# Performance work log

Hardware: AMD Instinct MI355X
Metric: run time of the kernel (lower is better)

## Reference

```python
import jax, jax.numpy as jnp
import numpy as np

VOCAB, HID, ADIM, B = 20, 128, 3, 32
NP, EP, NM, EM = 50000, 800000, 50000, 800000
IN_DIM = VOCAB + 3  # one-hot residues + 3D pos


def _gcn_conv(x, edge_index, W, b, n):
    # PyG GCNConv: h = XW; add self-loops; sym-normalized scatter-add; + bias
    h = x @ W
    loop = jnp.arange(n, dtype=edge_index.dtype)
    src = jnp.concatenate([edge_index[0], loop])
    dst = jnp.concatenate([edge_index[1], loop])
    deg = jax.ops.segment_sum(jnp.ones_like(dst, dtype=h.dtype), dst, num_segments=n)
    dinv = jnp.where(deg > 0, jax.lax.rsqrt(deg), 0.0)
    norm = dinv[src] * dinv[dst]  # [E+N]
    msg = h[src] * norm[:, None]  # [E+N, HID] dominant memory traffic
    return jax.ops.segment_sum(msg, dst, num_segments=n) + b


def _mean_pool(x, batch, nb):
    s = jax.ops.segment_sum(x, batch, num_segments=nb)
    c = jax.ops.segment_sum(jnp.ones((x.shape[0],), x.dtype), batch, num_segments=nb)
    return s / jnp.maximum(c, 1.0)[:, None]


def setup_inputs() -> dict:
    key = jax.random.key(0)
    ks = jax.random.split(key, 32)
    p = lambda k, shp: jax.random.normal(k, shp, dtype=jnp.float32) * 0.02
    inp = {
        "protein_residue": jax.random.randint(ks[0], (NP,), 0, VOCAB, dtype=jnp.int32),
        "protein_pos": jax.random.normal(ks[1], (NP, 3), dtype=jnp.float32),
        "protein_edge_index": jax.random.randint(ks[2], (2, EP), 0, NP, dtype=jnp.int32),
        "protein_batch": jnp.sort(jax.random.randint(ks[3], (NP,), 0, B, dtype=jnp.int32)),
        "molecule_residue": jax.random.randint(ks[4], (NM,), 0, VOCAB, dtype=jnp.int32),
        "molecule_pos": jax.random.normal(ks[5], (NM, 3), dtype=jnp.float32),
        "molecule_edge_index": jax.random.randint(ks[6], (2, EM), 0, NM, dtype=jnp.int32),
        "molecule_batch": jnp.sort(jax.random.randint(ks[7], (NM,), 0, B, dtype=jnp.int32)),
        "t": jax.random.randint(ks[8], (B,), 0, 1000, dtype=jnp.int32),
        "noisy_action": jax.random.normal(ks[9], (NM, ADIM), dtype=jnp.float32),
        # GCN params
        "Wp1": p(ks[10], (IN_DIM, HID)), "bp1": jnp.zeros((HID,), jnp.float32),
        "Wp2": p(ks[11], (HID, HID)),   "bp2": jnp.zeros((HID,), jnp.float32),
        "Wm1": p(ks[12], (IN_DIM, HID)), "bm1": jnp.zeros((HID,), jnp.float32),
        "Wm2": p(ks[13], (HID, HID)),   "bm2": jnp.zeros((HID,), jnp.float32),
        # timestep MLP
        "Wt1": p(ks[14], (1, HID)),   "bt1": jnp.zeros((HID,), jnp.float32),
        "Wt2": p(ks[15], (HID, HID)), "bt2": jnp.zeros((HID,), jnp.float32),
        # noise predictor: in = 2*HID + ADIM + HID = 387
        "Wn1": p(ks[16], (2 * HID + ADIM + HID, HID)), "bn1": jnp.zeros((HID,), jnp.float32),
        "Wn2": p(ks[17], (HID, ADIM)), "bn2": jnp.zeros((ADIM,), jnp.float32),
    }
    return inp


def reference(protein_residue, protein_pos, protein_edge_index, protein_batch,
              molecule_residue, molecule_pos, molecule_edge_index, molecule_batch,
              t, noisy_action,
              Wp1, bp1, Wp2, bp2, Wm1, bm1, Wm2, bm2,
              Wt1, bt1, Wt2, bt2, Wn1, bn1, Wn2, bn2):
    # protein branch
    x_p = jnp.concatenate([jax.nn.one_hot(protein_residue, VOCAB, dtype=jnp.float32), protein_pos], axis=1)
    x_p = jax.nn.relu(_gcn_conv(x_p, protein_edge_index, Wp1, bp1, NP))
    x_p = jax.nn.relu(_gcn_conv(x_p, protein_edge_index, Wp2, bp2, NP))
    protein_emb = _mean_pool(x_p, protein_batch, B)  # [B, HID]
    # molecule branch
    x_m = jnp.concatenate([jax.nn.one_hot(molecule_residue, VOCAB, dtype=jnp.float32), molecule_pos], axis=1)
    x_m = jax.nn.relu(_gcn_conv(x_m, molecule_edge_index, Wm1, bm1, NM))
    x_m = jax.nn.relu(_gcn_conv(x_m, molecule_edge_index, Wm2, bm2, NM))
    # timestep embedding
    t_emb = jax.nn.relu(t[:, None].astype(jnp.float32) @ Wt1 + bt1) @ Wt2 + bt2  # [B, HID]
    # gather pooled embeddings per molecule node, concat, MLP
    feat = jnp.concatenate([x_m, protein_emb[molecule_batch], t_emb[molecule_batch], noisy_action], axis=1)
    return jax.nn.relu(feat @ Wn1 + bn1) @ Wn2 + bn2  # [NM, ADIM]
```

## Files before the change

### kernel.cpp

```cpp
#include <hip/hip_runtime.h>
#include <hip/hip_bf16.h>

#define HID 128
#define BSH 7
#define CSRCAP 4096
#define PCHUNK 4096
#define HCHUNK 16384

typedef __attribute__((ext_vector_type(8))) short short8v;
typedef __attribute__((ext_vector_type(4))) float f32x4;

#if defined(__has_builtin)
#if __has_builtin(__builtin_amdgcn_cvt_f32_fp8) && __has_builtin(__builtin_amdgcn_cvt_pk_fp8_f32)
#define HAVE_HW_FP8 1
#endif
#endif

__device__ __forceinline__ float4 f4fma(float a, float4 x, float4 y) {
    y.x += a * x.x; y.y += a * x.y; y.z += a * x.z; y.w += a * x.w; return y;
}
__device__ __forceinline__ unsigned f2bf2(float lo, float hi) {
    unsigned ul = __float_as_uint(lo), uh = __float_as_uint(hi);
    ul = (ul + 0x7FFF + ((ul >> 16) & 1)) >> 16;
    uh = (uh + 0x7FFF + ((uh >> 16) & 1)) & 0xFFFF0000u;
    return ul | uh;
}
__device__ __forceinline__ unsigned short f2bf1(float v) {
    unsigned u = __float_as_uint(v);
    u = (u + 0x7FFF + ((u >> 16) & 1)) >> 16;
    return (unsigned short)u;
}
__device__ __forceinline__ float bflo(unsigned u) { return __uint_as_float(u << 16); }
__device__ __forceinline__ float bfhi(unsigned u) { return __uint_as_float(u & 0xFFFF0000u); }
__device__ __forceinline__ float bf2f(unsigned short b) {
    return __uint_as_float(((unsigned)b) << 16);
}
__device__ __forceinline__ short8v zero8() {
    short8v z = {0, 0, 0, 0, 0, 0, 0, 0};
    return z;
}

#ifndef HAVE_HW_FP8
__device__ __forceinline__ unsigned fp8enc_pos(float a) {
    if (a >= 448.f) return 0x7Eu;
    if (a < 0.0009765625f) return 0u;
    unsigned b = __float_as_uint(a);
    int e = (int)(b >> 23) - 127;
    if (e >= -6) {
        unsigned r = b + 0x7FFFFu + ((b >> 20) & 1u);
        e = (int)(r >> 23) - 127;
        unsigned m = (r >> 20) & 7u;
        return ((unsigned)(e + 7) << 3) | m;
    } else {
        int m = (int)(a * 512.f + 0.5f);
        return (unsigned)m;
    }
}
__device__ __forceinline__ float fp8dec1(unsigned u7) {
    float fn = __uint_as_float((u7 + 0x3C0u) << 20);
    float fs = (float)u7 * 0.001953125f;
    return u7 >= 8 ? fn : fs;
}
#endif

__device__ __forceinline__ unsigned char enc1(float a) {
#ifdef HAVE_HW_FP8
    return (unsigned char)(__builtin_amdgcn_cvt_pk_fp8_f32(a, 0.f, 0, false) & 0xff);
#else
    return (unsigned char)fp8enc_pos(a);
#endif
}
__device__ __forceinline__ void dec4(unsigned x, float* v) {
#ifdef HAVE_HW_FP8
    v[0] = __builtin_amdgcn_cvt_f32_fp8((int)x, 0);
    v[1] = __builtin_amdgcn_cvt_f32_fp8((int)x, 1);
    v[2] = __builtin_amdgcn_cvt_f32_fp8((int)x, 2);
    v[3] = __builtin_amdgcn_cvt_f32_fp8((int)x, 3);
#else
    v[0] = fp8dec1(x & 0xffu);         v[1] = fp8dec1((x >> 8) & 0xffu);
    v[2] = fp8dec1((x >> 16) & 0xffu); v[3] = fp8dec1(x >> 24);
#endif
}
__device__ __forceinline__ void dec16(uint4 u, float* v) {
    dec4(u.x, v); dec4(u.y, v + 4); dec4(u.z, v + 8); dec4(u.w, v + 12);
}

__global__ __launch_bounds__(256) void k_bhist(const int* __restrict__ d1, int e1,
        const int* __restrict__ d2, int e2, int base2,
        int* __restrict__ bktcnt, long etot) {
    __shared__ int hist[1024];
    int tid = threadIdx.x;
    for (int b = tid; b < 1024; b += 256) hist[b] = 0;
    __syncthreads();
    long start = (long)blockIdx.x * HCHUNK;
    long end = start + HCHUNK; if (end > etot) end = etot;
    for (long i = start + tid; i < end; i += 256) {
        int d = (i < e1) ? d1[i] : d2[i - e1] + base2;
        atomicAdd(&hist[d >> BSH], 1);
    }
    __syncthreads();
    for (int b = tid; b < 1024; b += 256)
        if (hist[b]) atomicAdd(&bktcnt[b], hist[b]);
}

__global__ void k_bscan(const int* __restrict__ bktcnt, int* __restrict__ bofs,
                        int* __restrict__ bcur) {
    __shared__ int s[1024];
    int tid = threadIdx.x;
    int v = bktcnt[tid];
    s[tid] = v; __syncthreads();
    for (int o = 1; o < 1024; o <<= 1) {
        int t = (tid >= o) ? s[tid - o] : 0;
        __syncthreads();
        s[tid] += t;
        __syncthreads();
    }
    int ex = s[tid] - v;
    bofs[tid] = ex;
    bcur[tid] = ex;
    if (tid == 1023) bofs[1024] = s[1023];
}

__global__ __launch_bounds__(256) void k_part(
        const int* __restrict__ s1, const int* __restrict__ d1, int e1,
        const int* __restrict__ s2, const int* __restrict__ d2, int e2, int base2,
        int* __restrict__ bcur, int* __restrict__ pedge, int nb, long etot) {
    __shared__ int hist[1024];
    __shared__ int lofs[1024];
    __shared__ int gb[1024];
    __shared__ int ps[256];
    __shared__ int stage[PCHUNK];
    __shared__ unsigned short sbk[PCHUNK];
    int tid = threadIdx.x;
    long cbase = (long)blockIdx.x * PCHUNK;
    int cnt = (int)((etot - cbase) < PCHUNK ? (etot - cbase) : PCHUNK);
    for (int b = tid; b < 1024; b += 256) hist[b] = 0;
    __syncthreads();
    for (int i = tid; i < cnt; i += 256) {
        long e = cbase + i;
        int d = (e < e1) ? d1[e] : d2[e - e1] + base2;
        atomicAdd(&hist[d >> BSH], 1);
    }
    __syncthreads();
    int h0 = hist[tid * 4], h1 = hist[tid * 4 + 1], h2 = hist[tid * 4 + 2], h3 = hist[tid * 4 + 3];
    int sum = h0 + h1 + h2 + h3;
    ps[tid] = sum; __syncthreads();
    for (int o = 1; o < 256; o <<= 1) {
        int v = (tid >= o) ? ps[tid - o] : 0;
        __syncthreads();
        ps[tid] += v;
        __syncthreads();
    }
    int ex = ps[tid] - sum;
    lofs[tid * 4] = ex; lofs[tid * 4 + 1] = ex + h0;
    lofs[tid * 4 + 2] = ex + h0 + h1; lofs[tid * 4 + 3] = ex + h0 + h1 + h2;
    __syncthreads();
    for (int b = tid; b < nb; b += 256) {
        int c = hist[b];
        gb[b] = c ? atomicAdd(&bcur[b], c) : 0;
    }
    __syncthreads();
    for (int b = tid; b < 1024; b += 256) hist[b] = 0;
    __syncthreads();
    for (int i = tid; i < cnt; i += 256) {
        long e = cbase + i;
        int s, d;
        if (e < e1) { s = s1[e]; d = d1[e]; }
        else { s = s2[e - e1] + base2; d = d2[e - e1] + base2; }
        int b = d >> BSH;
        int p = lofs[b] + atomicAdd(&hist[b], 1);
        stage[p] = (s << BSH) | (d & ((1 << BSH) - 1));
        sbk[p] = (unsigned short)b;
    }
    __syncthreads();
    for (int i = tid; i < cnt; i += 256) {
        int b = sbk[i];
        pedge[gb[b] + (i - lofs[b])] = stage[i];
    }
}

__global__ __launch_bounds__(256) void k_csr(const int* __restrict__ pe,
        const int* __restrict__ bofs, int* __restrict__ csrs,
        int* __restrict__ deg, int* __restrict__ offs, float* __restrict__ dinv,
        const int* __restrict__ res1, const float* __restrict__ pos1,
        const int* __restrict__ res2, const float* __restrict__ pos2,
        int np, int np64, uint4* __restrict__ nrec, int n) {
    __shared__ int lofs2[128];
    __shared__ int lcnt[128];
    __shared__ int lcur[128];
    __shared__ int sc[128];
    __shared__ int ss[CSRCAP];
    int b = blockIdx.x, tid = threadIdx.x;
    int n0 = b << BSH;
    int nn = (n - n0) < 128 ? (n - n0) : 128;
    if (tid < 128) { lcnt[tid] = 0; lcur[tid] = 0; }
    __syncthreads();
    int base = bofs[b], total = bofs[b + 1] - base;
    for (int i = tid; i < total; i += 256)
        atomicAdd(&lcnt[pe[base + i] & ((1 << BSH) - 1)], 1);
    __syncthreads();
    int v = 0;
    if (tid < 128) { v = lcnt[tid]; sc[tid] = v; }
    __syncthreads();
    for (int o = 1; o < 128; o <<= 1) {
        int t = 0;
        if (tid < 128 && tid >= o) t = sc[tid - o];
        __syncthreads();
        if (tid < 128) sc[tid] += t;
        __syncthreads();
    }
    if (tid < 128) lofs2[tid] = sc[tid] - v;
    if (tid < nn) {
        int node = n0 + tid;
        offs[node] = base + sc[tid] - v;
        deg[node] = v;
        float dv = rsqrtf((float)(v + 1));
        dinv[node] = dv;
        const int* res = 0; const float* pos = 0; int bseg = 0; bool valid = false;
        if (node < np) { res = res1; pos = pos1; bseg = 0; valid = true; }
        else if (node >= np64) { res = res2; pos = pos2; bseg = np64; valid = true; }
        if (valid) {
            int lg = node - bseg;
            uint4 rr;
            rr.x = __float_as_uint(dv);
            rr.y = (unsigned)res[lg] | ((unsigned)f2bf1(pos[lg * 3 + 0]) << 16);
            rr.z = (unsigned)f2bf1(pos[lg * 3 + 1]) | ((unsigned)f2bf1(pos[lg * 3 + 2]) << 16);
            rr.w = 0;
            nrec[node] = rr;
        }
    }
    __syncthreads();
    if (total <= CSRCAP) {
        for (int i = tid; i < total; i += 256) {
            int e = pe[base + i];
            int ln = e & ((1 << BSH) - 1);
            int pos_ = lofs2[ln] + atomicAdd(&lcur[ln], 1);
            ss[pos_] = e >> BSH;
        }
        __syncthreads();
        for (int i = tid; i < total; i += 256) csrs[base + i] = ss[i];
    } else {
        for (int i = tid; i < total; i += 256) {
            int e = pe[base + i];
            int ln = e & ((1 << BSH) - 1);
            int pos_ = lofs2[ln] + atomicAdd(&lcur[ln], 1);
            csrs[base + pos_] = e >> BSH;
        }
    }
}

__global__ __launch_bounds__(256) void k_agg23c(
        const uint4* __restrict__ nrec, const int* __restrict__ offs,
        const int* __restrict__ deg, const int* __restrict__ csrs,
        int np, int np64, int nm, unsigned short* __restrict__ x23) {
    __shared__ float aggL[8][21];
    int grp = threadIdx.x >> 5, lane = threadIdx.x & 31;
    int g = blockIdx.x * 8 + grp;
    int ntot = np64 + nm;
    if (g >= ntot) return;
    bool valid = (g < np) || (g >= np64);
    if (!valid) {
        if (lane < 16) ((unsigned*)x23)[(size_t)g * 16 + lane] = 0;
        return;
    }
    if (lane < 20) aggL[grp][lane] = 0.f;
    float sx = 0.f, sy = 0.f, sz = 0.f;
    int s0 = offs[g], m = deg[g];
    for (int i = lane; i < m; i += 32) {
        int s = csrs[s0 + i];
        uint4 r = nrec[s];
        float dv = __uint_as_float(r.x);
        int rs = (int)(r.y & 0xffffu);
        atomicAdd(&aggL[grp][rs], dv);
        sx += dv * bfhi(r.y); sy += dv * bflo(r.z); sz += dv * bfhi(r.z);
    }
    uint4 sr = nrec[g];
    float dd = __uint_as_float(sr.x);
    if (lane == 0) atomicAdd(&aggL[grp][(int)(sr.y & 0xffffu)], dd);
    #pragma unroll
    for (int o = 1; o < 32; o <<= 1) {
        sx += __shfl_xor(sx, o, 32);
        sy += __shfl_xor(sy, o, 32);
        sz += __shfl_xor(sz, o, 32);
    }
    sx += dd * bfhi(sr.y); sy += dd * bflo(sr.z); sz += dd * bfhi(sr.z);
    float val = 0.f;
    if (lane < 20) val = aggL[grp][lane];
    else if (lane == 20) val = sx;
    else if (lane == 21) val = sy;
    else if (lane == 22) val = sz;
    x23[(size_t)g * 32 + lane] = f2bf1(dd * val);
}

__global__ __launch_bounds__(256) void k_gemm1(const unsigned short* __restrict__ A,
        const unsigned short* __restrict__ Bt1, const unsigned short* __restrict__ Bt2,
        const float* __restrict__ b1a, const float* __restrict__ b1b,
        const float* __restrict__ dinv,
        int nb1, int np64, int ntot, unsigned* __restrict__ hb8) {
    __shared__ unsigned char stb[64][144];
    const int tid = threadIdx.x;
    const int wid = tid >> 6;
    const int lane = tid & 63;
    const int l15 = lane & 15, lg = lane >> 4;
    const unsigned short* Bt; const float* bb; int r0;
    if ((int)blockIdx.x < nb1) { Bt = Bt1; bb = b1a; r0 = blockIdx.x * 64; }
    else { Bt = Bt2; bb = b1b; r0 = np64 + ((int)blockIdx.x - nb1) * 64; }
    const int cbase = wid * 32;
    const int kb = lg * 8;
    f32x4 acc[4][2] = {};
    short8v b0 = *(const short8v*)&Bt[(size_t)(cbase + l15) * 32 + kb];
    short8v b1v = *(const short8v*)&Bt[(size_t)(cbase + 16 + l15) * 32 + kb];
    #pragma unroll
    for (int rt = 0; rt < 4; ++rt) {
        int gr = r0 + rt * 16 + l15;
        short8v a = (gr < ntot) ? *(const short8v*)&A[(size_t)gr * 32 + kb] : zero8();
        acc[rt][0] = __builtin_amdgcn_mfma_f32_16x16x32_bf16(a, b0, acc[rt][0], 0, 0, 0);
        acc[rt][1] = __builtin_amdgcn_mfma_f32_16x16x32_bf16(a, b1v, acc[rt][1], 0, 0, 0);
    }
    float bc0 = bb[cbase + l15], bc1 = bb[cbase + 16 + l15];
    #pragma unroll
    for (int rt = 0; rt < 4; ++rt)
        #pragma unroll
        for (int i = 0; i < 4; ++i) {
            int lr = rt * 16 + lg * 4 + i;
            int gr = r0 + lr;
            float dd16 = (gr < ntot) ? 16.f * dinv[gr] : 0.f;
            stb[lr][cbase + l15]      = enc1(dd16 * fmaxf(acc[rt][0][i] + bc0, 0.f));
            stb[lr][cbase + 16 + l15] = enc1(dd16 * fmaxf(acc[rt][1][i] + bc1, 0.f));
        }
    __syncthreads();
    #pragma unroll
    for (int h = 0; h < 2; ++h) {
        int idx = h * 256 + tid;
        int r = idx >> 3, q = idx & 7;
        int gr = r0 + r;
        if (gr < ntot)
            *(uint4*)&hb8[(size_t)gr * 32 + q * 4] = *(const uint4*)&stb[r][q * 16];
    }
}

__global__ __launch_bounds__(256) void k_agg(
        const uint4* __restrict__ H8, const int* __restrict__ offs,
        const int* __restrict__ deg, const int* __restrict__ csrs,
        const float* __restrict__ dinv,
        int np, int np64, int nm,
        unsigned short* __restrict__ outb) {
    int g = blockIdx.x * 8 + (threadIdx.x >> 5);
    if (g >= np && (g < np64 || g >= np64 + nm)) return;
    int lane = threadIdx.x & 31;
    int q = lane >> 3, l8 = lane & 7;
    float acc[16];
    if (q == 0) {
        uint4 u = H8[(size_t)g * 8 + l8];
        dec16(u, acc);
    } else {
        #pragma unroll
        for (int c = 0; c < 16; ++c) acc[c] = 0.f;
    }
    int s0 = offs[g], m = deg[g];
    for (int c0 = 0; c0 < m; c0 += 32) {
        int rem = m - c0; if (rem > 32) rem = 32;
        int li = lane < rem ? lane : rem - 1;
        int se = csrs[s0 + c0 + li];
        int nquad = (rem + 3) >> 2;
        #pragma unroll 8
        for (int j = 0; j < nquad; ++j) {
            int idx = j * 4 + q;
            bool act = idx < rem;
            int s = __shfl(se, act ? idx : 0, 32);
            uint4 u = H8[(size_t)s * 8 + l8];
            if (act) {
                float v[16]; dec16(u, v);
                #pragma unroll
                for (int c = 0; c < 16; ++c) acc[c] += v[c];
            }
        }
    }
    #pragma unroll
    for (int c = 0; c < 16; ++c) {
        acc[c] += __shfl_xor(acc[c], 8, 32);
        acc[c] += __shfl_xor(acc[c], 16, 32);
    }
    if (q == 0) {
        float di = dinv[g] * 0.0625f;
        uint4 pk0, pk1;
        pk0.x = f2bf2(di * acc[0],  di * acc[1]);
        pk0.y = f2bf2(di * acc[2],  di * acc[3]);
        pk0.z = f2bf2(di * acc[4],  di * acc[5]);
        pk0.w = f2bf2(di * acc[6],  di * acc[7]);
        pk1.x = f2bf2(di * acc[8],  di * acc[9]);
        pk1.y = f2bf2(di * acc[10], di * acc[11]);
        pk1.z = f2bf2(di * acc[12], di * acc[13]);
        pk1.w = f2bf2(di * acc[14], di * acc[15]);
        *(uint4*)&outb[(size_t)g * HID + l8 * 16]     = pk0;
        *(uint4*)&outb[(size_t)g * HID + l8 * 16 + 8] = pk1;
    }
}

__global__ void k_tr(const float* __restrict__ Wa, const float* __restrict__ Wb,
                     const float* __restrict__ Wc,
                     unsigned short* __restrict__ Ta, unsigned short* __restrict__ Tb,
                     unsigned short* __restrict__ Tc,
                     const float* __restrict__ W1a, const float* __restrict__ W1b,
                     unsigned short* __restrict__ T1a, unsigned short* __restrict__ T1b) {
    int b = blockIdx.x;
    int k = threadIdx.x;
    if (b < 384) {
        int col = b & 127, m = b >> 7;
        const float* W = (m == 0) ? Wa : (m == 1 ? Wb : Wc);
        unsigned short* T = (m == 0) ? Ta : (m == 1 ? Tb : Tc);
        T[col * HID + k] = f2bf1(W[k * HID + col]);
    } else {
        int bb = b - 384;
        int col = bb & 127, seg = bb >> 7;
        const float* W = seg ? W1b : W1a;
        unsigned short* T = seg ? T1b : T1a;
        if (k < 32) T[col * 32 + k] = (k < 23) ? f2bf1(W[k * HID + col]) : (unsigned short)0;
    }
}

__global__ __launch_bounds__(256) void k_gemm(const unsigned short* __restrict__ A,
        const unsigned short* __restrict__ Bt1, const unsigned short* __restrict__ Bt2,
        const float* __restrict__ b2a, const float* __restrict__ b2b,
        int nb1, int np64, int ntot, unsigned short* __restrict__ C) {
    const int tid = threadIdx.x;
    const int wid = tid >> 6;
    const int lane = tid & 63;
    const int l15 = lane & 15, lg = lane >> 4;
    const unsigned short* Bt; const float* bb; int r0;
    if ((int)blockIdx.x < nb1) { Bt = Bt1; bb = b2a; r0 = blockIdx.x * 64; }
    else { Bt = Bt2; bb = b2b; r0 = np64 + ((int)blockIdx.x - nb1) * 64; }
    const int cbase = wid * 32;
    f32x4 acc[4][2] = {};
    #pragma unroll
    for (int ks = 0; ks < 4; ++ks) {
        int kb = ks * 32 + lg * 8;
        short8v b0 = *(const short8v*)&Bt[(size_t)(cbase + l15) * HID + kb];
        short8v b1 = *(const short8v*)&Bt[(size_t)(cbase + 16 + l15) * HID + kb];
        #pragma unroll
        for (int rt = 0; rt < 4; ++rt) {
            int gr = r0 + rt * 16 + l15;
            short8v a = (gr < ntot) ? *(const short8v*)&A[(size_t)gr * HID + kb] : zero8();
            acc[rt][0] = __builtin_amdgcn_mfma_f32_16x16x32_bf16(a, b0, acc[rt][0], 0, 0, 0);
            acc[rt][1] = __builtin_amdgcn_mfma_f32_16x16x32_bf16(a, b1, acc[rt][1], 0, 0, 0);
        }
    }
    float bc0 = bb[cbase + l15], bc1 = bb[cbase + 16 + l15];
    #pragma unroll
    for (int rt = 0; rt < 4; ++rt)
        #pragma unroll
        for (int i = 0; i < 4; ++i) {
            int gr = r0 + rt * 16 + lg * 4 + i;
            if (gr < ntot) {
                C[(size_t)gr * HID + cbase + l15]      = f2bf1(fmaxf(acc[rt][0][i] + bc0, 0.f));
                C[(size_t)gr * HID + cbase + 16 + l15] = f2bf1(fmaxf(acc[rt][1][i] + bc1, 0.f));
            }
        }
}

__global__ void k_pool(const unsigned short* __restrict__ x, const int* __restrict__ batch,
                       float* __restrict__ pool, int* __restrict__ cnt, int n) {
    const int ROWS = 64;
    int start = blockIdx.x * ROWS;
    if (start >= n) return;
    int end = start + ROWS; if (end > n) end = n;
    int c = threadIdx.x;
    float acc = 0.f;
    int cur = batch[start];
    int run = 0;
    for (int r = start; r < end; ++r) {
        int b = batch[r];
        if (b != cur) {
            atomicAdd(&pool[cur * HID + c], acc);
            if (c == 0) atomicAdd(&cnt[cur], run);
            acc = 0.f; run = 0; cur = b;
        }
        acc += bf2f(x[(size_t)r * HID + c]);
        run++;
    }
    atomicAdd(&pool[cur * HID + c], acc);
    if (c == 0) atomicAdd(&cnt[cur], run);
}

__global__ void k_combo2(const int* __restrict__ t, const float* __restrict__ Wt1,
                         const float* __restrict__ bt1, const float* __restrict__ Wt2,
                         const float* __restrict__ bt2,
                         const float* __restrict__ pool, const int* __restrict__ cntb,
                         const float* __restrict__ Wn1, const float* __restrict__ bn1,
                         float* __restrict__ combo) {
    __shared__ float th[HID];
    __shared__ float pe[HID];
    __shared__ float te[HID];
    int b = blockIdx.x, c = threadIdx.x;
    float tv = (float)t[b];
    float hv = tv * Wt1[c] + bt1[c];
    th[c] = hv > 0.f ? hv : 0.f;
    float dcnt = (float)cntb[b]; if (dcnt < 1.f) dcnt = 1.f;
    pe[c] = pool[b * HID + c] / dcnt;
    __syncthreads();
    float s = bt2[c];
    for (int k = 0; k < HID; ++k) s += th[k] * Wt2[k * HID + c];
    te[c] = s;
    __syncthreads();
    const float* Wp = Wn1 + 128 * HID;
    const float* Wt = Wn1 + 256 * HID;
    float o = bn1[c];
    for (int k = 0; k < HID; ++k)
        o += pe[k] * Wp[k * HID + c] + te[k] * Wt[k * HID + c];
    combo[b * HID + c] = o;
}

__global__ __launch_bounds__(256) void k_final(const unsigned short* __restrict__ A,
        const unsigned short* __restrict__ Bt ,
        const float* __restrict__ Wn1, const float* __restrict__ combo,
        const int* __restrict__ mbatch, const float* __restrict__ noisy,
        const float* __restrict__ Wn2, const float* __restrict__ bn2,
        float* __restrict__ out, int n) {
    __shared__ float hsm[64][132];
    const int tid = threadIdx.x;
    const int wid = tid >> 6;
    const int lane = tid & 63;
    const int l15 = lane & 15, lg = lane >> 4;
    const int r0 = blockIdx.x * 64;
    const int cbase = wid * 32;
    f32x4 acc[4][2] = {};
    #pragma unroll
    for (int ks = 0; ks < 4; ++ks) {
        int kb = ks * 32 + lg * 8;
        short8v b0 = *(const short8v*)&Bt[(size_t)(cbase + l15) * HID + kb];
        short8v b1 = *(const short8v*)&Bt[(size_t)(cbase + 16 + l15) * HID + kb];
        #pragma unroll
        for (int rt = 0; rt < 4; ++rt) {
            int gr = r0 + rt * 16 + l15;
            short8v a = (gr < n) ? *(const short8v*)&A[(size_t)gr * HID + kb] : zero8();
            acc[rt][0] = __builtin_amdgcn_mfma_f32_16x16x32_bf16(a, b0, acc[rt][0], 0, 0, 0);
            acc[rt][1] = __builtin_amdgcn_mfma_f32_16x16x32_bf16(a, b1, acc[rt][1], 0, 0, 0);
        }
    }
    const float* Wna = Wn1 + 384 * HID;
    #pragma unroll
    for (int rt = 0; rt < 4; ++rt)
        #pragma unroll
        for (int i = 0; i < 4; ++i) {
            int lr = rt * 16 + lg * 4 + i;
            int gr = r0 + lr;
            if (gr < n) {
                int b = mbatch[gr];
                float na0 = noisy[gr * 3 + 0], na1 = noisy[gr * 3 + 1], na2 = noisy[gr * 3 + 2];
                #pragma unroll
                for (int ct = 0; ct < 2; ++ct) {
                    int col = cbase + ct * 16 + l15;
                    float v = acc[rt][ct][i]
                            + na0 * Wna[col] + na1 * Wna[HID + col] + na2 * Wna[2 * HID + col]
                            + combo[b * HID + col];
                    hsm[lr][col] = v > 0.f ? v : 0.f;
                }
            }
        }
    __syncthreads();
    if (tid < 192) {
        int lr = tid / 3, j = tid - lr * 3;
        int gr = r0 + lr;
        if (gr < n) {
            float s = bn2[j];
            for (int c = 0; c < HID; ++c) s += hsm[lr][c] * Wn2[c * 3 + j];
            out[(size_t)gr * 3 + j] = s;
        }
    }
}

extern "C" void kernel_launch(void* const* d_in, const int* in_sizes, int n_in,
                              void* d_out, int out_size, void* d_ws, size_t ws_size,
                              hipStream_t stream) {
    const int*   p_res  = (const int*)d_in[0];
    const float* p_pos  = (const float*)d_in[1];
    const int*   p_ei   = (const int*)d_in[2];
    const int*   p_bat  = (const int*)d_in[3];
    const int*   m_res  = (const int*)d_in[4];
    const float* m_pos  = (const float*)d_in[5];
    const int*   m_ei   = (const int*)d_in[6];
    const int*   m_bat  = (const int*)d_in[7];
    const int*   t      = (const int*)d_in[8];
    const float* noisy  = (const float*)d_in[9];
    const float* Wp1 = (const float*)d_in[10], *bp1 = (const float*)d_in[11];
    const float* Wp2 = (const float*)d_in[12], *bp2 = (const float*)d_in[13];
    const float* Wm1 = (const float*)d_in[14], *bm1 = (const float*)d_in[15];
    const float* Wm2 = (const float*)d_in[16], *bm2 = (const float*)d_in[17];
    const float* Wt1 = (const float*)d_in[18], *bt1 = (const float*)d_in[19];
    const float* Wt2 = (const float*)d_in[20], *bt2 = (const float*)d_in[21];
    const float* Wn1 = (const float*)d_in[22], *bn1 = (const float*)d_in[23];
    const float* Wn2 = (const float*)d_in[24], *bn2 = (const float*)d_in[25];
    float* out = (float*)d_out;

    const int NP = in_sizes[0];
    const int EP = in_sizes[2] / 2;
    const int NM = in_sizes[4];
    const int EM = in_sizes[6] / 2;
    const int B  = in_sizes[8];
    auto al64 = [](int x) { return (x + 63) & ~63; };

    const int np64 = al64(NP);
    const long ntot_m = (long)np64 + NM;
    const long e2sum = (long)EP + EM;

    auto align256 = [](size_t x) { return (x + 255) & ~(size_t)255; };
    size_t req = 0;
    auto count = [&](size_t nb) { req = align256(req) + nb; };
    count(4ull * ntot_m);
    count(4ull * ntot_m);
    count(4ull * ntot_m);
    count(16ull * ntot_m);
    count(4ull * (1024 + 1025 + 1024));
    count(4ull * e2sum);
    count(4ull * e2sum);
    count(1ull * ntot_m * HID);
    count(2ull * ntot_m * HID);
    count(2ull * ntot_m * HID);
    count(2ull * (3 * HID * HID + 2 * HID * 32));
    count(4ull * (size_t)B * (HID + 1));
    count(4ull * (size_t)B * HID);
    bool merged = ws_size >= req + 4096;

    char* ws = (char*)d_ws;
    size_t off = 0;
    auto alloc = [&](size_t nb) { off = align256(off); size_t r = off; off += nb; return r; };

    const int NMAX = NP > NM ? NP : NM;
    const int EMAXs = EP > EM ? EP : EM;
    const long ntot_a = merged ? ntot_m : (long)al64(NMAX);
    const long etot_a = merged ? e2sum : (long)EMAXs;

    int*   deg  = (int*)(ws + alloc(4ull * ntot_a));
    int*   offs = (int*)(ws + alloc(4ull * ntot_a));
    float* dinv = (float*)(ws + alloc(4ull * ntot_a));
    uint4* nrec = (uint4*)(ws + alloc(16ull * ntot_a));
    int*   bktcnt = (int*)(ws + alloc(4ull * (1024 + 1025 + 1024)));
    int*   bofs = bktcnt + 1024;
    int*   bcur = bofs + 1025;
    int*   csre = (int*)(ws + alloc(4ull * etot_a));
    int*   csrs = (int*)(ws + alloc(4ull * etot_a));
    unsigned* hb8 = (unsigned*)(ws + alloc(1ull * ntot_a * HID));
    unsigned short* hb = (unsigned short*)(ws + alloc(2ull * ntot_a * HID));
    unsigned short* hc = (unsigned short*)(ws + alloc(2ull * ntot_a * HID));
    unsigned short* x23 = hc;
    unsigned short* w2ta = (unsigned short*)(ws + alloc(2ull * (3 * HID * HID + 2 * HID * 32)));
    unsigned short* w2tb = w2ta + HID * HID;
    unsigned short* wn1t = w2ta + 2 * HID * HID;
    unsigned short* w1ta = w2ta + 3 * HID * HID;
    unsigned short* w1tb = w1ta + HID * 32;
    float* pool = (float*)(ws + alloc(4ull * (size_t)B * (HID + 1)));
    int*   cntb = (int*)(pool + (size_t)B * HID);
    float* combo = (float*)(ws + alloc(4ull * (size_t)B * HID));

    k_tr<<<640, HID, 0, stream>>>(Wp2, Wm2, Wn1, w2ta, w2tb, wn1t, Wp1, Wm1, w1ta, w1tb);

    auto run = [&](int np_, int nm_,
                   const int* ei1, int e1, const int* ei2, int e2,
                   const int* res1, const float* pos1, const int* res2, const float* pos2,
                   const float* b1a, const float* b1b,
                   const unsigned short* w1A, const unsigned short* w1B,
                   const float* b2a, const float* b2b) {
        const int np64_ = al64(np_);
        const int ntot = np64_ + nm_;
        const long etot = (long)e1 + e2;
        const int nb = (ntot + 127) >> BSH;
        const int* s1 = ei1, *d1 = ei1 + e1;
        const int* s2 = ei2, *d2 = ei2 + e2;
        hipMemsetAsync(bktcnt, 0, 4096, stream);
        k_bhist<<<(int)((etot + HCHUNK - 1) / HCHUNK), 256, 0, stream>>>(
            d1, e1, d2, e2, np64_, bktcnt, etot);
        k_bscan<<<1, 1024, 0, stream>>>(bktcnt, bofs, bcur);
        k_part<<<(int)((etot + PCHUNK - 1) / PCHUNK), 256, 0, stream>>>(
            s1, d1, e1, s2, d2, e2, np64_, bcur, csre, nb, etot);
        k_csr<<<nb, 256, 0, stream>>>(csre, bofs, csrs, deg, offs, dinv,
                                      res1, pos1, res2, pos2, np_, np64_, nrec, ntot);
        k_agg23c<<<(ntot + 7) / 8, 256, 0, stream>>>(nrec, offs, deg, csrs,
                                                     np_, np64_, nm_, x23);
        const int nb1 = np64_ / 64;
        const int nb2 = (nm_ + 63) / 64;
        k_gemm1<<<nb1 + nb2, 256, 0, stream>>>(x23, w1A, w1B, b1a, b1b, dinv,
                                               nb1, np64_, ntot, hb8);
        k_agg<<<(ntot + 7) / 8, 256, 0, stream>>>((const uint4*)hb8, offs, deg, csrs, dinv,
                                                  np_, np64_, nm_, hc);
        k_gemm<<<nb1 + nb2, 256, 0, stream>>>(hc, w2ta, w2tb, b2a, b2b, nb1, np64_, ntot, hb);
    };

    if (merged) {
        run(NP, NM, p_ei, EP, m_ei, EM,
            p_res, p_pos, m_res, m_pos,
            bp1, bm1, w1ta, w1tb, bp2, bm2);
        hipMemsetAsync(pool, 0, 4ull * (size_t)B * (HID + 1), stream);
        k_pool<<<(NP + 63) / 64, HID, 0, stream>>>(hb, p_bat, pool, cntb, NP);
        k_combo2<<<B, HID, 0, stream>>>(t, Wt1, bt1, Wt2, bt2, pool, cntb, Wn1, bn1, combo);
        k_final<<<(NM + 63) / 64, 256, 0, stream>>>(hb + (size_t)np64 * HID, wn1t, Wn1, combo,
                                                    m_bat, noisy, Wn2, bn2, out, NM);
    } else {
        run(NP, 0, p_ei, EP, p_ei, 0,
            p_res, p_pos, p_res, p_pos,
            bp1, bp1, w1ta, w1ta, bp2, bp2);
        hipMemsetAsync(pool, 0, 4ull * (size_t)B * (HID + 1), stream);
        k_pool<<<(NP + 63) / 64, HID, 0, stream>>>(hb, p_bat, pool, cntb, NP);
        k_combo2<<<B, HID, 0, stream>>>(t, Wt1, bt1, Wt2, bt2, pool, cntb, Wn1, bn1, combo);
        run(0, NM, m_ei, 0, m_ei, EM,
            m_res, m_pos, m_res, m_pos,
            bm1, bm1, w1tb, w1tb, bm2, bm2);
        k_final<<<(NM + 63) / 64, 256, 0, stream>>>(hb, wn1t, Wn1, combo, m_bat, noisy,
                                                    Wn2, bn2, out, NM);
    }
}
```

Before: 228.8 us.

## Fold bucket-count memset into kernels, pack FP8 decode, split LDS atomics

Drops the hipMemsetAsync of the bucket histogram and instead zeroes it inside k_tr before first use and at the end of k_csr for any later run. Replaces the per-byte FP8 decode in the aggregation kernel with packed two-at-a-time conversion into float2 accumulators. Splits the shared-memory residue histogram in k_agg23c into two half-wave copies to reduce atomic contention. Zeroing inside k_csr depends on bktcnt no longer being read after k_bscan, and the packed builtin must be present or the fallback path is compiled.

After: 225.3 us. Within noise of the previous version (-1.5%).

```diff
diff --git a/kernel.cpp b/kernel.cpp
--- a/kernel.cpp
+++ b/kernel.cpp
@@ -9,10 +9,14 @@
 
 typedef __attribute__((ext_vector_type(8))) short short8v;
 typedef __attribute__((ext_vector_type(4))) float f32x4;
+typedef __attribute__((ext_vector_type(2))) float f32x2;
 
 #if defined(__has_builtin)
 #if __has_builtin(__builtin_amdgcn_cvt_f32_fp8) && __has_builtin(__builtin_amdgcn_cvt_pk_fp8_f32)
 #define HAVE_HW_FP8 1
+#endif
+#if __has_builtin(__builtin_amdgcn_cvt_pk_f32_fp8)
+#define HAVE_HW_FP8_PK 1
 #endif
 #endif
 
@@ -70,19 +74,27 @@
     return (unsigned char)fp8enc_pos(a);
 #endif
 }
-__device__ __forceinline__ void dec4(unsigned x, float* v) {
-#ifdef HAVE_HW_FP8
-    v[0] = __builtin_amdgcn_cvt_f32_fp8((int)x, 0);
-    v[1] = __builtin_amdgcn_cvt_f32_fp8((int)x, 1);
-    v[2] = __builtin_amdgcn_cvt_f32_fp8((int)x, 2);
-    v[3] = __builtin_amdgcn_cvt_f32_fp8((int)x, 3);
+
+__device__ __forceinline__ void dec16p(uint4 u, f32x2* v) {
+#ifdef HAVE_HW_FP8_PK
+    v[0] = __builtin_amdgcn_cvt_pk_f32_fp8((int)u.x, false);
+    v[1] = __builtin_amdgcn_cvt_pk_f32_fp8((int)u.x, true);
+    v[2] = __builtin_amdgcn_cvt_pk_f32_fp8((int)u.y, false);
+    v[3] = __builtin_amdgcn_cvt_pk_f32_fp8((int)u.y, true);
+    v[4] = __builtin_amdgcn_cvt_pk_f32_fp8((int)u.z, false);
+    v[5] = __builtin_amdgcn_cvt_pk_f32_fp8((int)u.z, true);
+    v[6] = __builtin_amdgcn_cvt_pk_f32_fp8((int)u.w, false);
+    v[7] = __builtin_amdgcn_cvt_pk_f32_fp8((int)u.w, true);
 #else
-    v[0] = fp8dec1(x & 0xffu);         v[1] = fp8dec1((x >> 8) & 0xffu);
-    v[2] = fp8dec1((x >> 16) & 0xffu); v[3] = fp8dec1(x >> 24);
+    unsigned w[4] = {u.x, u.y, u.z, u.w};
+    #pragma unroll
+    for (int k = 0; k < 4; ++k) {
+        f32x2 a, b;
+        a.x = fp8dec1(w[k] & 0xffu);         a.y = fp8dec1((w[k] >> 8) & 0xffu);
+        b.x = fp8dec1((w[k] >> 16) & 0xffu); b.y = fp8dec1(w[k] >> 24);
+        v[2 * k] = a; v[2 * k + 1] = b;
+    }
 #endif
-}
-__device__ __forceinline__ void dec16(uint4 u, float* v) {
-    dec4(u.x, v); dec4(u.y, v + 4); dec4(u.z, v + 8); dec4(u.w, v + 12);
 }
 
 __global__ __launch_bounds__(256) void k_bhist(const int* __restrict__ d1, int e1,
@@ -184,7 +196,7 @@
         int* __restrict__ deg, int* __restrict__ offs, float* __restrict__ dinv,
         const int* __restrict__ res1, const float* __restrict__ pos1,
         const int* __restrict__ res2, const float* __restrict__ pos2,
-        int np, int np64, uint4* __restrict__ nrec, int n) {
+        int np, int np64, uint4* __restrict__ nrec, int n, int* __restrict__ bktcnt) {
     __shared__ int lofs2[128];
     __shared__ int lcnt[128];
     __shared__ int lcur[128];
@@ -247,13 +259,15 @@
             csrs[base + pos_] = e >> BSH;
         }
     }
+    if (b == 0)
+        for (int i = tid; i < 1024; i += 256) bktcnt[i] = 0;
 }
 
 __global__ __launch_bounds__(256) void k_agg23c(
         const uint4* __restrict__ nrec, const int* __restrict__ offs,
         const int* __restrict__ deg, const int* __restrict__ csrs,
         int np, int np64, int nm, unsigned short* __restrict__ x23) {
-    __shared__ float aggL[8][21];
+    __shared__ float aggL[8][2][24];
     int grp = threadIdx.x >> 5, lane = threadIdx.x & 31;
     int g = blockIdx.x * 8 + grp;
     int ntot = np64 + nm;
@@ -263,7 +277,8 @@
         if (lane < 16) ((unsigned*)x23)[(size_t)g * 16 + lane] = 0;
         return;
     }
-    if (lane < 20) aggL[grp][lane] = 0.f;
+    int hf = lane >> 4;
+    if (lane < 20) { aggL[grp][0][lane] = 0.f; aggL[grp][1][lane] = 0.f; }
     float sx = 0.f, sy = 0.f, sz = 0.f;
     int s0 = offs[g], m = deg[g];
     for (int i = lane; i < m; i += 32) {
@@ -271,12 +286,12 @@
         uint4 r = nrec[s];
         float dv = __uint_as_float(r.x);
         int rs = (int)(r.y & 0xffffu);
-        atomicAdd(&aggL[grp][rs], dv);
+        atomicAdd(&aggL[grp][hf][rs], dv);
         sx += dv * bfhi(r.y); sy += dv * bflo(r.z); sz += dv * bfhi(r.z);
     }
     uint4 sr = nrec[g];
     float dd = __uint_as_float(sr.x);
-    if (lane == 0) atomicAdd(&aggL[grp][(int)(sr.y & 0xffffu)], dd);
+    if (lane == 0) atomicAdd(&aggL[grp][0][(int)(sr.y & 0xffffu)], dd);
     #pragma unroll
     for (int o = 1; o < 32; o <<= 1) {
         sx += __shfl_xor(sx, o, 32);
@@ -285,7 +300,7 @@
     }
     sx += dd * bfhi(sr.y); sy += dd * bflo(sr.z); sz += dd * bfhi(sr.z);
     float val = 0.f;
-    if (lane < 20) val = aggL[grp][lane];
+    if (lane < 20) val = aggL[grp][0][lane] + aggL[grp][1][lane];
     else if (lane == 20) val = sx;
     else if (lane == 21) val = sy;
     else if (lane == 22) val = sz;
@@ -349,13 +364,13 @@
     if (g >= np && (g < np64 || g >= np64 + nm)) return;
     int lane = threadIdx.x & 31;
     int q = lane >> 3, l8 = lane & 7;
-    float acc[16];
+    f32x2 acc2[8];
     if (q == 0) {
         uint4 u = H8[(size_t)g * 8 + l8];
-        dec16(u, acc);
+        dec16p(u, acc2);
     } else {
         #pragma unroll
-        for (int c = 0; c < 16; ++c) acc[c] = 0.f;
+        for (int c = 0; c < 8; ++c) { acc2[c].x = 0.f; acc2[c].y = 0.f; }
     }
     int s0 = offs[g], m = deg[g];
     for (int c0 = 0; c0 < m; c0 += 32) {
@@ -370,28 +385,30 @@
             int s = __shfl(se, act ? idx : 0, 32);
             uint4 u = H8[(size_t)s * 8 + l8];
             if (act) {
-                float v[16]; dec16(u, v);
+                f32x2 v[8]; dec16p(u, v);
                 #pragma unroll
-                for (int c = 0; c < 16; ++c) acc[c] += v[c];
+                for (int c = 0; c < 8; ++c) acc2[c] += v[c];
             }
         }
     }
     #pragma unroll
-    for (int c = 0; c < 16; ++c) {
-        acc[c] += __shfl_xor(acc[c], 8, 32);
-        acc[c] += __shfl_xor(acc[c], 16, 32);
+    for (int c = 0; c < 8; ++c) {
+        acc2[c].x += __shfl_xor(acc2[c].x, 8, 32);
+        acc2[c].y += __shfl_xor(acc2[c].y, 8, 32);
+        acc2[c].x += __shfl_xor(acc2[c].x, 16, 32);
+        acc2[c].y += __shfl_xor(acc2[c].y, 16, 32);
     }
     if (q == 0) {
         float di = dinv[g] * 0.0625f;
         uint4 pk0, pk1;
-        pk0.x = f2bf2(di * acc[0],  di * acc[1]);
-        pk0.y = f2bf2(di * acc[2],  di * acc[3]);
-        pk0.z = f2bf2(di * acc[4],  di * acc[5]);
-        pk0.w = f2bf2(di * acc[6],  di * acc[7]);
-        pk1.x = f2bf2(di * acc[8],  di * acc[9]);
-        pk1.y = f2bf2(di * acc[10], di * acc[11]);
-        pk1.z = f2bf2(di * acc[12], di * acc[13]);
-        pk1.w = f2bf2(di * acc[14], di * acc[15]);
+        pk0.x = f2bf2(di * acc2[0].x, di * acc2[0].y);
+        pk0.y = f2bf2(di * acc2[1].x, di * acc2[1].y);
+        pk0.z = f2bf2(di * acc2[2].x, di * acc2[2].y);
+        pk0.w = f2bf2(di * acc2[3].x, di * acc2[3].y);
+        pk1.x = f2bf2(di * acc2[4].x, di * acc2[4].y);
+        pk1.y = f2bf2(di * acc2[5].x, di * acc2[5].y);
+        pk1.z = f2bf2(di * acc2[6].x, di * acc2[6].y);
+        pk1.w = f2bf2(di * acc2[7].x, di * acc2[7].y);
         *(uint4*)&outb[(size_t)g * HID + l8 * 16]     = pk0;
         *(uint4*)&outb[(size_t)g * HID + l8 * 16 + 8] = pk1;
     }
@@ -402,9 +419,12 @@
                      unsigned short* __restrict__ Ta, unsigned short* __restrict__ Tb,
                      unsigned short* __restrict__ Tc,
                      const float* __restrict__ W1a, const float* __restrict__ W1b,
-                     unsigned short* __restrict__ T1a, unsigned short* __restrict__ T1b) {
+                     unsigned short* __restrict__ T1a, unsigned short* __restrict__ T1b,
+                     int* __restrict__ bktcnt) {
     int b = blockIdx.x;
     int k = threadIdx.x;
+    if (b == 0)
+        for (int i = k; i < 1024; i += HID) bktcnt[i] = 0;
     if (b < 384) {
         int col = b & 127, m = b >> 7;
         const float* W = (m == 0) ? Wa : (m == 1 ? Wb : Wc);
@@ -652,7 +672,8 @@
     int*   cntb = (int*)(pool + (size_t)B * HID);
     float* combo = (float*)(ws + alloc(4ull * (size_t)B * HID));
 
-    k_tr<<<640, HID, 0, stream>>>(Wp2, Wm2, Wn1, w2ta, w2tb, wn1t, Wp1, Wm1, w1ta, w1tb);
+    k_tr<<<640, HID, 0, stream>>>(Wp2, Wm2, Wn1, w2ta, w2tb, wn1t, Wp1, Wm1, w1ta, w1tb,
+                                  bktcnt);
 
     auto run = [&](int np_, int nm_,
                    const int* ei1, int e1, const int* ei2, int e2,
@@ -666,14 +687,13 @@
         const int nb = (ntot + 127) >> BSH;
         const int* s1 = ei1, *d1 = ei1 + e1;
         const int* s2 = ei2, *d2 = ei2 + e2;
-        hipMemsetAsync(bktcnt, 0, 4096, stream);
         k_bhist<<<(int)((etot + HCHUNK - 1) / HCHUNK), 256, 0, stream>>>(
             d1, e1, d2, e2, np64_, bktcnt, etot);
         k_bscan<<<1, 1024, 0, stream>>>(bktcnt, bofs, bcur);
         k_part<<<(int)((etot + PCHUNK - 1) / PCHUNK), 256, 0, stream>>>(
             s1, d1, e1, s2, d2, e2, np64_, bcur, csre, nb, etot);
         k_csr<<<nb, 256, 0, stream>>>(csre, bofs, csrs, deg, offs, dinv,
-                                      res1, pos1, res2, pos2, np_, np64_, nrec, ntot);
+                                      res1, pos1, res2, pos2, np_, np64_, nrec, ntot, bktcnt);
         k_agg23c<<<(ntot + 7) / 8, 256, 0, stream>>>(nrec, offs, deg, csrs,
                                                      np_, np64_, nm_, x23);
         const int nb1 = np64_ / 64;
```
